# Kernel optimization log

Hardware: AMD Instinct MI355X
Metric: run time of the kernel (lower is better)

Reference implementation:

```python
import jax, jax.numpy as jnp
import numpy as np

B, N, D = 8, 2048, 512
DIM_ATTN, DIM_VAL = 512, 512


def setup_inputs() -> dict:
    key = jax.random.key(0)
    ks = jax.random.split(key, 7)
    s = 1.0 / np.sqrt(D)
    return {
        "x": jax.random.normal(ks[0], (B, N, D), dtype=jnp.float32),
        "Wq": jax.random.normal(ks[1], (D, DIM_ATTN), dtype=jnp.float32) * s,
        "bq": jnp.zeros((DIM_ATTN,), dtype=jnp.float32),
        "Wk": jax.random.normal(ks[2], (D, DIM_ATTN), dtype=jnp.float32) * s,
        "bk": jnp.zeros((DIM_ATTN,), dtype=jnp.float32),
        "Wv": jax.random.normal(ks[3], (D, DIM_VAL), dtype=jnp.float32) * s,
        "bv": jnp.zeros((DIM_VAL,), dtype=jnp.float32),
    }


def reference(x, Wq, bq, Wk, bk, Wv, bv):
    # relu-activated dense projections (Keras Dense with relu)
    Q = jax.nn.relu(jnp.einsum("bnd,de->bne", x, Wq) + bq)  # [B,N,dim_attn]
    K = jax.nn.relu(jnp.einsum("bnd,de->bne", x, Wk) + bk)  # [B,N,dim_attn]
    V = jax.nn.relu(jnp.einsum("bnd,de->bne", x, Wv) + bv)  # [B,N,dim_val]
    scale = 1.0 / jnp.sqrt(jnp.asarray(Q.shape[-1], dtype=jnp.float32))
    scores = jnp.einsum("bqe,bke->bqk", Q, K) * scale       # [B,N,N]
    attn = jax.nn.softmax(scores, axis=-1)
    return jnp.einsum("bqk,bkv->bqv", attn, V)               # [B,N,dim_val]
```

## Files before the change

kernel.cpp:

```cpp
#include <hip/hip_runtime.h>
#include <stdint.h>

typedef _Float16 f16;
typedef __attribute__((ext_vector_type(8))) _Float16 f16x8;
typedef __attribute__((ext_vector_type(4))) float f32x4;

#define QSCALE 0.0637587159f

__device__ __forceinline__ void gload16(const void* g, void* l) {
  __builtin_amdgcn_global_load_lds(
      (const __attribute__((address_space(1))) unsigned int*)(uintptr_t)g,
      (__attribute__((address_space(3))) unsigned int*)(uintptr_t)l,
      16, 0, 0);
}

__global__ __launch_bounds__(256) void k_cvt_x(const float* __restrict__ x,
                                               f16* __restrict__ xb) {
  const int i = (blockIdx.x * 256 + threadIdx.x) * 8;
  const float4 a = *(const float4*)(x + i);
  const float4 b = *(const float4*)(x + i + 4);
  f16x8 o;
  o[0] = (f16)a.x; o[1] = (f16)a.y; o[2] = (f16)a.z; o[3] = (f16)a.w;
  o[4] = (f16)b.x; o[5] = (f16)b.y; o[6] = (f16)b.z; o[7] = (f16)b.w;
  *(f16x8*)(xb + i) = o;
}

__global__ __launch_bounds__(256) void k_tw(const float* __restrict__ Wq,
                                            const float* __restrict__ Wk,
                                            const float* __restrict__ Wv,
                                            f16* __restrict__ Wqkt,
                                            f16* __restrict__ Wvt) {
  const int t = blockIdx.x * 256 + threadIdx.x;
  const int mat = t >> 16;
  const int rem = t & 65535;
  const int e = rem & 511;
  const int d4 = (rem >> 9) << 2;
  const float* W = (mat == 0) ? Wq : (mat == 1 ? Wk : Wv);
  f16* dst = (mat == 0) ? (Wqkt + e * 512)
           : (mat == 1 ? (Wqkt + (512 + e) * 512) : (Wvt + e * 512));
#pragma unroll
  for (int i = 0; i < 4; i++) dst[d4 + i] = (f16)W[(d4 + i) * 512 + e];
}

__device__ __forceinline__ void gemm_tile(const f16* __restrict__ Ag,
                                          const f16* __restrict__ Btg,
                                          f32x4 acc[4][4]) {
  __shared__ __align__(16) f16 As[128 * 64];
  __shared__ __align__(16) f16 Bs[128 * 64];
  const int lane = threadIdx.x & 63;
  const int w = threadIdx.x >> 6;
  const int wr = (w >> 1) * 64;
  const int wc = (w & 1) * 64;
#pragma unroll
  for (int i = 0; i < 4; i++)
#pragma unroll
    for (int j = 0; j < 4; j++) acc[i][j] = (f32x4){0.f, 0.f, 0.f, 0.f};

  for (int kt = 0; kt < 8; ++kt) {
#pragma unroll
    for (int i = 0; i < 4; i++) {
      const int r = w * 32 + i * 8 + (lane >> 3);
      const int src = kt * 64 + (((lane & 7) * 8) ^ ((r & 7) << 3));
      gload16(Ag + r * 512 + src, &As[(w * 32 + i * 8) * 64]);
      gload16(Btg + r * 512 + src, &Bs[(w * 32 + i * 8) * 64]);
    }
    __syncthreads();
#pragma unroll
    for (int ks = 0; ks < 2; ++ks) {
      f16x8 a[4], bfr[4];
#pragma unroll
      for (int i = 0; i < 4; i++) {
        const int row = wr + i * 16 + (lane & 15);
        a[i] = *(const f16x8*)&As[row * 64 +
                 ((ks * 32 + 8 * (lane >> 4)) ^ ((row & 7) << 3))];
      }
#pragma unroll
      for (int j = 0; j < 4; j++) {
        const int row = wc + j * 16 + (lane & 15);
        bfr[j] = *(const f16x8*)&Bs[row * 64 +
                 ((ks * 32 + 8 * (lane >> 4)) ^ ((row & 7) << 3))];
      }
#pragma unroll
      for (int i = 0; i < 4; i++)
#pragma unroll
        for (int j = 0; j < 4; j++)
          acc[i][j] = __builtin_amdgcn_mfma_f32_16x16x32_f16(a[i], bfr[j],
                                                             acc[i][j], 0, 0, 0);
    }
    __syncthreads();
  }
}

__global__ __launch_bounds__(256) void k_qk_proj(
    const f16* __restrict__ xb, const f16* __restrict__ Wqkt,
    const float* __restrict__ bq, const float* __restrict__ bk,
    f16* __restrict__ Q, f16* __restrict__ K) {
  const int rt = blockIdx.x, ct = blockIdx.y;
  f32x4 acc[4][4];
  gemm_tile(xb + rt * 128 * 512, Wqkt + ct * 128 * 512, acc);
  const int lane = threadIdx.x & 63;
  const int w = threadIdx.x >> 6;
  const int wr = (w >> 1) * 64, wc = (w & 1) * 64;
  const bool isQ = (ct < 4);
  const float* bias = isQ ? bq : bk;
  f16* dst = isQ ? Q : K;
  const int cb = (ct & 3) * 128;
  const float qs = isQ ? QSCALE : 1.0f;
#pragma unroll
  for (int j = 0; j < 4; j++) {
    const int col = cb + wc + j * 16 + (lane & 15);
    const float bb = bias[col];
#pragma unroll
    for (int i = 0; i < 4; i++) {
      const int nbase = rt * 128 + wr + i * 16 + 4 * (lane >> 4);
#pragma unroll
      for (int r = 0; r < 4; r++) {
        float v = fmaxf(acc[i][j][r] + bb, 0.f) * qs;
        dst[(nbase + r) * 512 + col] = (f16)v;
      }
    }
  }
}

__global__ __launch_bounds__(256) void k_v_proj(
    const f16* __restrict__ Wvt, const f16* __restrict__ xb,
    const float* __restrict__ bv, f16* __restrict__ Vt) {
  const int rt = blockIdx.x;
  const int ct = blockIdx.y;
  f32x4 acc[4][4];
  gemm_tile(Wvt + rt * 128 * 512, xb + ct * 128 * 512, acc);
  const int lane = threadIdx.x & 63;
  const int w = threadIdx.x >> 6;
  const int wr = (w >> 1) * 64, wc = (w & 1) * 64;
#pragma unroll
  for (int i = 0; i < 4; i++) {
    const int ebase = rt * 128 + wr + i * 16 + 4 * (lane >> 4);
#pragma unroll
    for (int j = 0; j < 4; j++) {
      const int n = ct * 128 + wc + j * 16 + (lane & 15);
      const int b = n >> 11, nb = n & 2047;
#pragma unroll
      for (int r = 0; r < 4; r++) {
        const int e = ebase + r;
        float v = fmaxf(acc[i][j][r] + bv[e], 0.f);
        Vt[(b * 512 + e) * 2048 + nb] = (f16)v;
      }
    }
  }
}

__global__ __launch_bounds__(256) void k_attn(
    const f16* __restrict__ Q, const f16* __restrict__ K,
    const f16* __restrict__ Vt, float* __restrict__ out) {
  __shared__ __align__(16) f16 smem[70144];
  const int b = blockIdx.x & 7;
  const int qb = blockIdx.x >> 3;
  const int lane = threadIdx.x & 63;
  const int w = threadIdx.x >> 6;
  const f16* Qg = Q + (b * 2048 + qb * 64) * 512;
  const f16* Kg = K + b * 2048 * 512;
  const f16* Vg = Vt + b * 512 * 2048;
  f16* const Ps = smem + 65536;

#pragma unroll
  for (int i = 0; i < 16; i++) {
    const int r = w * 16 + i;
    const int src = (lane * 8) ^ ((r & 7) << 3);
    gload16(Qg + r * 512 + src, &smem[r * 512]);
  }
  __syncthreads();
  f16x8 qf[16];
  {
    const int row = w * 16 + (lane & 15);
#pragma unroll
    for (int ks = 0; ks < 16; ++ks)
      qf[ks] = *(const f16x8*)&smem[row * 512 +
               ((ks * 32 + 8 * (lane >> 4)) ^ ((row & 7) << 3))];
  }
  __syncthreads();

#pragma unroll
  for (int i = 0; i < 8; i++) {
    const int r = w * 8 + i;
    gload16(Kg + r * 512 + ((lane * 8) ^ ((r & 7) << 3)), smem + r * 512);
  }
#pragma unroll
  for (int i = 0; i < 8; i++) {
    const int row = w * 128 + i * 16 + (lane >> 2);
    const int col = (8 * (lane & 3)) ^ (8 * ((row >> 1) & 3));
    gload16(Vg + row * 2048 + col, smem + 32768 + (w * 128 + i * 16) * 32);
  }
  __syncthreads();

  f32x4 o[32];
#pragma unroll
  for (int i = 0; i < 32; i++) o[i] = (f32x4){0.f, 0.f, 0.f, 0.f};
  float m[4] = {-1e30f, -1e30f, -1e30f, -1e30f};
  float l[4] = {0.f, 0.f, 0.f, 0.f};
  int cur = 0;

  for (int kt = 0; kt < 64; ++kt) {
    if (kt < 63) {
      const f16* Kgn = Kg + (kt + 1) * 32 * 512;
      const f16* Vgn = Vg + (kt + 1) * 32;
      f16* kd = smem + (cur ^ 1) * 16384;
      f16* vd = smem + 32768 + (cur ^ 1) * 16384;
#pragma unroll
      for (int i = 0; i < 8; i++) {
        const int r = w * 8 + i;
        gload16(Kgn + r * 512 + ((lane * 8) ^ ((r & 7) << 3)), kd + r * 512);
      }
#pragma unroll
      for (int i = 0; i < 8; i++) {
        const int row = w * 128 + i * 16 + (lane >> 2);
        const int col = (8 * (lane & 3)) ^ (8 * ((row >> 1) & 3));
        gload16(Vgn + row * 2048 + col, vd + (w * 128 + i * 16) * 32);
      }
    }
    const f16* Ks = smem + cur * 16384;
    const f16* Vs = smem + 32768 + cur * 16384;

    f32x4 s[2];
#pragma unroll
    for (int c = 0; c < 2; c++) s[c] = (f32x4){0.f, 0.f, 0.f, 0.f};
#pragma unroll
    for (int ks = 0; ks < 16; ++ks) {
#pragma unroll
      for (int c = 0; c < 2; c++) {
        const int row = c * 16 + (lane & 15);
        const f16x8 kf = *(const f16x8*)&Ks[row * 512 +
                        ((ks * 32 + 8 * (lane >> 4)) ^ ((row & 7) << 3))];
        s[c] = __builtin_amdgcn_mfma_f32_16x16x32_f16(qf[ks], kf, s[c], 0, 0, 0);
      }
    }

    float sc[4];
#pragma unroll
    for (int r = 0; r < 4; r++) {
      float v = fmaxf(s[0][r], s[1][r]);
      v = fmaxf(v, __shfl_xor(v, 1));
      v = fmaxf(v, __shfl_xor(v, 2));
      v = fmaxf(v, __shfl_xor(v, 4));
      v = fmaxf(v, __shfl_xor(v, 8));
      const float nm = fmaxf(m[r], v);
      sc[r] = exp2f(m[r] - nm);
      m[r] = nm;
      float rs = 0.f;
      const int prow = 4 * (lane >> 4) + r;
#pragma unroll
      for (int c = 0; c < 2; c++) {
        const float pv = exp2f(s[c][r] - nm);
        Ps[w * 1152 + prow * 72 + c * 16 + (lane & 15)] = (f16)pv;
        rs += pv;
      }
      rs += __shfl_xor(rs, 1);
      rs += __shfl_xor(rs, 2);
      rs += __shfl_xor(rs, 4);
      rs += __shfl_xor(rs, 8);
      l[r] = l[r] * sc[r] + rs;
    }
    {
      const f32x4 scv = {sc[0], sc[1], sc[2], sc[3]};
#pragma unroll
      for (int i = 0; i < 32; i++) o[i] *= scv;
    }

    const f16x8 pf = *(const f16x8*)&Ps[w * 1152 + (lane & 15) * 72 +
                                        8 * (lane >> 4)];
#pragma unroll
    for (int dt = 0; dt < 32; ++dt) {
      const int row = dt * 16 + (lane & 15);
      const f16x8 v0 = *(const f16x8*)&Vs[row * 32 +
                      ((8 * (lane >> 4)) ^ (8 * ((row >> 1) & 3)))];
      o[dt] = __builtin_amdgcn_mfma_f32_16x16x32_f16(pf, v0, o[dt], 0, 0, 0);
    }
    __syncthreads();
    cur ^= 1;
  }

  float rl[4];
#pragma unroll
  for (int r = 0; r < 4; r++) rl[r] = 1.0f / l[r];
  float* ob = out + ((b * 2048 + qb * 64 + w * 16 + 4 * (lane >> 4)) * 512) + (lane & 15);
#pragma unroll
  for (int dt = 0; dt < 32; ++dt)
#pragma unroll
    for (int r = 0; r < 4; r++)
      ob[r * 512 + dt * 16] = o[dt][r] * rl[r];
}

extern "C" void kernel_launch(void* const* d_in, const int* in_sizes, int n_in,
                              void* d_out, int out_size, void* d_ws, size_t ws_size,
                              hipStream_t stream) {
  const float* x  = (const float*)d_in[0];
  const float* Wq = (const float*)d_in[1];
  const float* bq = (const float*)d_in[2];
  const float* Wk = (const float*)d_in[3];
  const float* bk = (const float*)d_in[4];
  const float* Wv = (const float*)d_in[5];
  const float* bv = (const float*)d_in[6];
  float* out = (float*)d_out;
  char* ws = (char*)d_ws;

  f16* xb   = (f16*)(ws);
  f16* Wqkt = (f16*)(ws + 16777216);
  f16* Wvt  = (f16*)(ws + 16777216 + 1048576);
  f16* Qb   = (f16*)(ws + 18350080);
  f16* Kb   = (f16*)(ws + 18350080 + 16777216);
  f16* Vtb  = (f16*)(ws + 18350080 + 2 * 16777216);

  hipLaunchKernelGGL(k_cvt_x, dim3(4096), dim3(256), 0, stream, x, xb);
  hipLaunchKernelGGL(k_tw, dim3(768), dim3(256), 0, stream, Wq, Wk, Wv, Wqkt, Wvt);
  hipLaunchKernelGGL(k_qk_proj, dim3(128, 8), dim3(256), 0, stream, xb, Wqkt, bq, bk, Qb, Kb);
  hipLaunchKernelGGL(k_v_proj, dim3(4, 128), dim3(256), 0, stream, Wvt, xb, bv, Vtb);
  hipLaunchKernelGGL(k_attn, dim3(256), dim3(256), 0, stream, Qb, Kb, Vtb, out);
}
```

Before: 328.4 us.

## Split attention KV sequence across two wave groups with in-block merge

```diff
diff --git a/kernel.cpp b/kernel.cpp
--- a/kernel.cpp
+++ b/kernel.cpp
@@ -149,29 +149,32 @@
   }
 }
 
-__global__ __launch_bounds__(256) void k_attn(
+__global__ __launch_bounds__(512, 2) void k_attn(
     const f16* __restrict__ Q, const f16* __restrict__ K,
     const f16* __restrict__ Vt, float* __restrict__ out) {
-  __shared__ __align__(16) f16 smem[70144];
+  __shared__ __align__(16) f16 smem[74752];
   const int b = blockIdx.x & 7;
   const int qb = blockIdx.x >> 3;
   const int lane = threadIdx.x & 63;
   const int w = threadIdx.x >> 6;
+  const int grp = w >> 2;
+  const int wq = w & 3;
   const f16* Qg = Q + (b * 2048 + qb * 64) * 512;
   const f16* Kg = K + b * 2048 * 512;
   const f16* Vg = Vt + b * 512 * 2048;
-  f16* const Ps = smem + 65536;
-
-#pragma unroll
-  for (int i = 0; i < 16; i++) {
-    const int r = w * 16 + i;
-    const int src = (lane * 8) ^ ((r & 7) << 3);
-    gload16(Qg + r * 512 + src, &smem[r * 512]);
+  f16* const Ps = smem + 65536 + w * 1152;
+  f16* const Ks = smem + grp * 16384;
+  f16* const Vs = smem + 32768 + grp * 16384;
+
+#pragma unroll
+  for (int i = 0; i < 8; i++) {
+    const int r = w * 8 + i;
+    gload16(Qg + r * 512 + ((lane * 8) ^ ((r & 7) << 3)), &smem[r * 512]);
   }
   __syncthreads();
   f16x8 qf[16];
   {
-    const int row = w * 16 + (lane & 15);
+    const int row = wq * 16 + (lane & 15);
 #pragma unroll
     for (int ks = 0; ks < 16; ++ks)
       qf[ks] = *(const f16x8*)&smem[row * 512 +
@@ -179,16 +182,20 @@
   }
   __syncthreads();
 
-#pragma unroll
-  for (int i = 0; i < 8; i++) {
-    const int r = w * 8 + i;
-    gload16(Kg + r * 512 + ((lane * 8) ^ ((r & 7) << 3)), smem + r * 512);
-  }
-#pragma unroll
-  for (int i = 0; i < 8; i++) {
-    const int row = w * 128 + i * 16 + (lane >> 2);
-    const int col = (8 * (lane & 3)) ^ (8 * ((row >> 1) & 3));
-    gload16(Vg + row * 2048 + col, smem + 32768 + (w * 128 + i * 16) * 32);
+  {
+    const int t = grp;
+#pragma unroll
+    for (int i = 0; i < 8; i++) {
+      const int r = wq * 8 + i;
+      gload16(Kg + (t * 32 + r) * 512 + ((lane * 8) ^ ((r & 7) << 3)),
+              Ks + r * 512);
+    }
+#pragma unroll
+    for (int i = 0; i < 8; i++) {
+      const int row = wq * 128 + i * 16 + (lane >> 2);
+      const int col = (8 * (lane & 3)) ^ (8 * ((row >> 1) & 3));
+      gload16(Vg + row * 2048 + t * 32 + col, Vs + (wq * 128 + i * 16) * 32);
+    }
   }
   __syncthreads();
 
@@ -197,29 +204,8 @@
   for (int i = 0; i < 32; i++) o[i] = (f32x4){0.f, 0.f, 0.f, 0.f};
   float m[4] = {-1e30f, -1e30f, -1e30f, -1e30f};
   float l[4] = {0.f, 0.f, 0.f, 0.f};
-  int cur = 0;
-
-  for (int kt = 0; kt < 64; ++kt) {
-    if (kt < 63) {
-      const f16* Kgn = Kg + (kt + 1) * 32 * 512;
-      const f16* Vgn = Vg + (kt + 1) * 32;
-      f16* kd = smem + (cur ^ 1) * 16384;
-      f16* vd = smem + 32768 + (cur ^ 1) * 16384;
-#pragma unroll
-      for (int i = 0; i < 8; i++) {
-        const int r = w * 8 + i;
-        gload16(Kgn + r * 512 + ((lane * 8) ^ ((r & 7) << 3)), kd + r * 512);
-      }
-#pragma unroll
-      for (int i = 0; i < 8; i++) {
-        const int row = w * 128 + i * 16 + (lane >> 2);
-        const int col = (8 * (lane & 3)) ^ (8 * ((row >> 1) & 3));
-        gload16(Vgn + row * 2048 + col, vd + (w * 128 + i * 16) * 32);
-      }
-    }
-    const f16* Ks = smem + cur * 16384;
-    const f16* Vs = smem + 32768 + cur * 16384;
-
+
+  for (int p = 0; p < 32; ++p) {
     f32x4 s[2];
 #pragma unroll
     for (int c = 0; c < 2; c++) s[c] = (f32x4){0.f, 0.f, 0.f, 0.f};
@@ -250,7 +236,7 @@
 #pragma unroll
       for (int c = 0; c < 2; c++) {
         const float pv = exp2f(s[c][r] - nm);
-        Ps[w * 1152 + prow * 72 + c * 16 + (lane & 15)] = (f16)pv;
+        Ps[prow * 72 + c * 16 + (lane & 15)] = (f16)pv;
         rs += pv;
       }
       rs += __shfl_xor(rs, 1);
@@ -265,8 +251,7 @@
       for (int i = 0; i < 32; i++) o[i] *= scv;
     }
 
-    const f16x8 pf = *(const f16x8*)&Ps[w * 1152 + (lane & 15) * 72 +
-                                        8 * (lane >> 4)];
+    const f16x8 pf = *(const f16x8*)&Ps[(lane & 15) * 72 + 8 * (lane >> 4)];
 #pragma unroll
     for (int dt = 0; dt < 32; ++dt) {
       const int row = dt * 16 + (lane & 15);
@@ -274,19 +259,69 @@
                       ((8 * (lane >> 4)) ^ (8 * ((row >> 1) & 3)))];
       o[dt] = __builtin_amdgcn_mfma_f32_16x16x32_f16(pf, v0, o[dt], 0, 0, 0);
     }
-    __syncthreads();
-    cur ^= 1;
-  }
-
-  float rl[4];
-#pragma unroll
-  for (int r = 0; r < 4; r++) rl[r] = 1.0f / l[r];
-  float* ob = out + ((b * 2048 + qb * 64 + w * 16 + 4 * (lane >> 4)) * 512) + (lane & 15);
-#pragma unroll
-  for (int dt = 0; dt < 32; ++dt)
-#pragma unroll
-    for (int r = 0; r < 4; r++)
-      ob[r * 512 + dt * 16] = o[dt][r] * rl[r];
+
+    if (p < 31) {
+      __syncthreads();
+      const int t = 2 * (p + 1) + grp;
+#pragma unroll
+      for (int i = 0; i < 8; i++) {
+        const int r = wq * 8 + i;
+        gload16(Kg + (t * 32 + r) * 512 + ((lane * 8) ^ ((r & 7) << 3)),
+                Ks + r * 512);
+      }
+#pragma unroll
+      for (int i = 0; i < 8; i++) {
+        const int row = wq * 128 + i * 16 + (lane >> 2);
+        const int col = (8 * (lane & 3)) ^ (8 * ((row >> 1) & 3));
+        gload16(Vg + row * 2048 + t * 32 + col, Vs + (wq * 128 + i * 16) * 32);
+      }
+      __syncthreads();
+    }
+  }
+
+  __syncthreads();
+  float* const obuf = (float*)smem;
+  float* const mlbuf = (float*)(smem + 65536);
+  if (grp == 0) {
+    if ((lane & 15) == 0) {
+#pragma unroll
+      for (int r = 0; r < 4; r++) {
+        const int row = wq * 16 + 4 * (lane >> 4) + r;
+        mlbuf[row] = m[r];
+        mlbuf[64 + row] = l[r];
+      }
+    }
+#pragma unroll
+    for (int dt = 0; dt < 32; ++dt) {
+      const int idx = wq * 8192 + (dt * 16 + (lane & 15)) * 16 + 4 * (lane >> 4);
+      *(f32x4*)&obuf[idx] = o[dt];
+    }
+  }
+  __syncthreads();
+  if (grp == 1) {
+    f32x4 fAv, fBv;
+#pragma unroll
+    for (int r = 0; r < 4; r++) {
+      const int row = wq * 16 + 4 * (lane >> 4) + r;
+      const float m1 = mlbuf[row], l1 = mlbuf[64 + row];
+      const float M = fmaxf(m1, m[r]);
+      const float a = exp2f(m1 - M);
+      const float bb = exp2f(m[r] - M);
+      const float rv = 1.0f / (l1 * a + l[r] * bb);
+      fAv[r] = a * rv;
+      fBv[r] = bb * rv;
+    }
+    float* ob = out + ((b * 2048 + qb * 64 + wq * 16 + 4 * (lane >> 4)) * 512) +
+                (lane & 15);
+#pragma unroll
+    for (int dt = 0; dt < 32; ++dt) {
+      const int idx = wq * 8192 + (dt * 16 + (lane & 15)) * 16 + 4 * (lane >> 4);
+      const f32x4 o1v = *(const f32x4*)&obuf[idx];
+      const f32x4 res = o1v * fAv + o[dt] * fBv;
+#pragma unroll
+      for (int r = 0; r < 4; r++) ob[r * 512 + dt * 16] = res[r];
+    }
+  }
 }
 
 extern "C" void kernel_launch(void* const* d_in, const int* in_sizes, int n_in,
@@ -313,5 +348,5 @@
   hipLaunchKernelGGL(k_tw, dim3(768), dim3(256), 0, stream, Wq, Wk, Wv, Wqkt, Wvt);
   hipLaunchKernelGGL(k_qk_proj, dim3(128, 8), dim3(256), 0, stream, xb, Wqkt, bq, bk, Qb, Kb);
   hipLaunchKernelGGL(k_v_proj, dim3(4, 128), dim3(256), 0, stream, Wvt, xb, bv, Vtb);
-  hipLaunchKernelGGL(k_attn, dim3(256), dim3(256), 0, stream, Qb, Kb, Vtb, out);
-}
+  hipLaunchKernelGGL(k_attn, dim3(256), dim3(512), 0, stream, Qb, Kb, Vtb, out);
+}
```

Result: slower. 418.1 us (+27.3%).
